# Optimization experiments

Measured on AMD Instinct MI355X. Metric: run time of the kernel, lower is better.

## Reference

```python
import jax, jax.numpy as jnp
import numpy as np

NUM_HEADS = 8
GROUP_SIZE = 4
INF = 1000000.0


def _group(x, mask, g):
    # x: [N, L, D] -> [N, L//g, D] (mean over group); mask: any over group
    N, L, D = x.shape
    xg = x.reshape(N, L // g, g, D).mean(axis=2)
    mg = mask.reshape(N, L // g, g).any(axis=2)
    return xg, mg


def _heads(x, h):
    N, L, D = x.shape
    return x.reshape(N, L, h, D // h)


def _alpha(logits, mask_row, mask_col):
    # logits: [N, L1, L2, H]; masks: [N, L1], [N, L2] (same across heads)
    pair = (mask_row[:, :, None] & mask_col[:, None, :])[..., None]  # [N,L1,L2,1]
    logits = jnp.where(pair, logits, logits - INF)
    alpha = jax.nn.softmax(logits, axis=2)
    return jnp.where(mask_row[:, :, None, None], alpha, jnp.zeros_like(alpha))


def setup_inputs() -> dict:
    key = jax.random.key(0)
    ks = jax.random.split(key, 9)
    N, Lp, Ls, D = 32, 4096, 1024, 256
    protein = jax.random.normal(ks[0], (N, Lp, D), dtype=jnp.float32)
    sm = jax.random.normal(ks[1], (N, Ls, D), dtype=jnp.float32)
    mask_prot = jax.random.randint(ks[2], (N, Lp), 0, 2) > 0
    mask_sm = jax.random.randint(ks[3], (N, Ls), 0, 2) > 0
    scale = 1.0 / np.sqrt(D)
    Wk_p = jax.random.normal(ks[4], (D, D), dtype=jnp.float32) * scale
    Wv_p = jax.random.normal(ks[5], (D, D), dtype=jnp.float32) * scale
    Wq_d = jax.random.normal(ks[6], (D, D), dtype=jnp.float32) * scale
    Wk_d = jax.random.normal(ks[7], (D, D), dtype=jnp.float32) * scale
    Wv_d = jax.random.normal(ks[8], (D, D), dtype=jnp.float32) * scale
    return {"protein": protein, "sm": sm, "mask_prot": mask_prot,
            "mask_sm": mask_sm, "Wk_p": Wk_p, "Wv_p": Wv_p,
            "Wq_d": Wq_d, "Wk_d": Wk_d, "Wv_d": Wv_d}


def reference(protein, sm, mask_prot, mask_sm, Wk_p, Wv_p, Wq_d, Wk_d, Wv_d):
    H = NUM_HEADS
    prot_g, mprot_g = _group(protein, mask_prot, GROUP_SIZE)
    sm_g, msm_g = _group(sm, mask_sm, GROUP_SIZE)

    key_prot = _heads(prot_g @ Wk_p, H)   # [N, Gp, H, d]
    val_prot = _heads(prot_g @ Wv_p, H)
    query_sm = _heads(sm_g @ Wq_d, H)     # [N, Gs, H, d]
    key_sm = _heads(sm_g @ Wk_d, H)
    val_sm = _heads(sm_g @ Wv_d, H)

    logits_dp = jnp.einsum('blhd,bkhd->blkh', query_sm, key_prot)
    logits_dd = jnp.einsum('blhd,bkhd->blkh', query_sm, key_sm)

    alpha_dp = _alpha(logits_dp, msm_g, mprot_g)
    alpha_dd = _alpha(logits_dd, msm_g, msm_g)

    out_dp = jnp.einsum('blkh,bkhd->blhd', alpha_dp, val_prot)
    out_dd = jnp.einsum('blkh,bkhd->blhd', alpha_dd, val_sm)
    N, Gs = out_dp.shape[0], out_dp.shape[1]
    return (out_dp.reshape(N, Gs, -1) + out_dd.reshape(N, Gs, -1)) * 0.5
```

## Files before the change

### kernel.cpp

```cpp
#include <hip/hip_runtime.h>
#include <cstdint>
#include <cstddef>

#define N_B 32
#define D_MODEL 256
#define H_N 8
#define HD 32
#define GP 1024
#define GS 256
#define LOG2E 1.4426950408889634f

typedef __attribute__((ext_vector_type(8))) _Float16 half8;
typedef __attribute__((ext_vector_type(4))) float floatx4;

#if __has_builtin(__builtin_amdgcn_exp2f)
#define EXP2(x) __builtin_amdgcn_exp2f(x)
#else
#define EXP2(x) exp2f(x)
#endif

__device__ __forceinline__ unsigned short f2h(float f) {
    _Float16 h = (_Float16)f;
    return __builtin_bit_cast(unsigned short, h);
}

__device__ __forceinline__ unsigned pack_h_rne(float a, float b) {
    return (unsigned)f2h(a) | ((unsigned)f2h(b) << 16);
}

#define PRO_A (N_B * GP * 64)
#define PRO_B (N_B * GS * 64)
#define PRO_C (N_B * GP)
#define PRO_D (N_B * GS)
#define PRO_BLOCKS ((PRO_A + PRO_B + PRO_C + PRO_D) / 256)
#define WT_BLOCKS 80
__global__ __launch_bounds__(256) void prologue_w(
        const float4* __restrict__ prot, const float4* __restrict__ smx,
        const int* __restrict__ mp, const int* __restrict__ ms,
        ushort4* __restrict__ prot_g, ushort4* __restrict__ sm_g,
        float* __restrict__ bias_p, float* __restrict__ bias_s,
        const float* __restrict__ Wk_p, const float* __restrict__ Wv_p,
        const float* __restrict__ Wq_d, const float* __restrict__ Wk_d,
        const float* __restrict__ Wv_d,
        unsigned short* __restrict__ WTbig, unsigned short* __restrict__ WTsml) {
    __shared__ unsigned short sT[64 * 65];
    int blk = blockIdx.x;
    int t = threadIdx.x;
    if (blk >= WT_BLOCKS) {
        int gid = (blk - WT_BLOCKS) * 256 + t;
        if (gid < PRO_A + PRO_B) {
            const float4* x; ushort4* xg; int g2;
            if (gid < PRO_A) { x = prot; xg = prot_g; g2 = gid; }
            else { x = smx; xg = sm_g; g2 = gid - PRO_A; }
            int row = g2 >> 6, c = g2 & 63;
            const float4* p = x + (size_t)row * 256 + c;
            float4 a = p[0], b = p[64], cc = p[128], d = p[192];
            ushort4 r;
            r.x = f2h(0.25f * (a.x + b.x + cc.x + d.x));
            r.y = f2h(0.25f * (a.y + b.y + cc.y + d.y));
            r.z = f2h(0.25f * (a.z + b.z + cc.z + d.z));
            r.w = f2h(0.25f * (a.w + b.w + cc.w + d.w));
            xg[g2] = r;
        } else {
            int g2 = gid - (PRO_A + PRO_B);
            const int* m; float* bias;
            if (g2 < PRO_C) { m = mp; bias = bias_p; }
            else { m = ms; bias = bias_s; g2 -= PRO_C; }
            const int* p = m + (size_t)g2 * 4;
            bias[g2] = (p[0] | p[1] | p[2] | p[3]) ? 0.0f : -1442695.0f;
        }
    } else {
        int wb = blk;
        int y = wb >> 4, bx = wb & 15;
        const float* W; unsigned short* WT; int pidx;
        if (y < 2) { W = (y == 0) ? Wk_p : Wv_p; WT = WTbig; pidx = y; }
        else {
            int q = y - 2;
            W = (q == 0) ? Wq_d : (q == 1 ? Wk_d : Wv_d);
            WT = WTsml; pidx = q;
        }
        int kt = bx >> 2, ct = bx & 3;
        int k0 = kt * 64, c0 = ct * 64;
#pragma unroll
        for (int j = 0; j < 4; j++) {
            int idx = j * 256 + t;
            int kr = idx >> 4, cf = idx & 15;
            float4 v = *(const float4*)&W[(size_t)(k0 + kr) * 256 + c0 + cf * 4];
            sT[(cf * 4 + 0) * 65 + kr] = f2h(v.x);
            sT[(cf * 4 + 1) * 65 + kr] = f2h(v.y);
            sT[(cf * 4 + 2) * 65 + kr] = f2h(v.z);
            sT[(cf * 4 + 3) * 65 + kr] = f2h(v.w);
        }
        __syncthreads();
#pragma unroll
        for (int j = 0; j < 8; j++) {
            int idx = j * 256 + t;
            int cw = idx >> 5, kq = idx & 31;
            unsigned lo = sT[cw * 65 + kq * 2];
            unsigned hi = sT[cw * 65 + kq * 2 + 1];
            ((unsigned*)WT)[((size_t)pidx * 256 + c0 + cw) * 128 + (k0 >> 1) + kq] =
                lo | (hi << 16);
        }
    }
}

__global__ __launch_bounds__(256) void gemm_f16(
        const unsigned short* __restrict__ Abig,
        const unsigned short* __restrict__ WTbig,
        const unsigned short* __restrict__ Asml,
        const unsigned short* __restrict__ WTsml,
        unsigned short* __restrict__ Kp, unsigned short* __restrict__ Vpt,
        unsigned short* __restrict__ Qd, unsigned short* __restrict__ Ksd,
        unsigned short* __restrict__ Vsdt) {
    __shared__ alignas(16) unsigned short lds[128 * 128];
    unsigned short* As = lds;
    unsigned short* Bs = lds + 8192;

    int bid = blockIdx.x;
    int id = (bid & 7) * 176 + (bid >> 3);

    const unsigned short *A, *WT;
    unsigned short *oK0, *oK1, *oV;
    int Gg, lgG, row0, col0;
    float scale0;
    bool isV;
    if (id < 1024) {
        A = Abig; WT = WTbig; oK0 = Kp; oK1 = Kp; oV = Vpt;
        Gg = GP; lgG = 10; scale0 = 1.0f;
        col0 = (id & 3) << 7; row0 = (id >> 2) << 7;
        isV = (col0 >= 256);
    } else {
        int tq = id - 1024;
        A = Asml; WT = WTsml; oK0 = Qd; oK1 = Ksd; oV = Vsdt;
        Gg = GS; lgG = 8; scale0 = LOG2E;
        col0 = (tq % 6) << 7; row0 = (tq / 6) << 7;
        isV = (col0 >= 512);
    }
    const int tid = threadIdx.x;
    const int ln = tid & 63, wave = tid >> 6;
    const int m16 = ln & 15, quad = ln >> 4;
    const int wm = (wave & 1) * 64, wn = (wave >> 1) * 64;

    const uint4* gA[4];
    const uint4* gB[4];
    unsigned ldsoff[4];
#pragma unroll
    for (int j = 0; j < 4; j++) {
        int u = (j * 4 + wave) * 64 + ln;
        int r = u >> 3, s = u & 7;
        int sg = (s - r) & 7;
        gA[j] = (const uint4*)A + (size_t)(row0 + r) * 32 + sg;
        gB[j] = (const uint4*)WT + (size_t)(col0 + r) * 32 + sg;
        ldsoff[j] = (unsigned)((j * 4 + wave) * 512);
    }
    int aaddr[4], baddr[4];
#pragma unroll
    for (int i = 0; i < 4; i++) {
        int rA = wm + i * 16 + m16;
        aaddr[i] = rA * 128 + ((quad + rA) & 7) * 16;
        int rB = wn + i * 16 + m16;
        baddr[i] = rB * 128 + ((quad + rB) & 7) * 16;
    }

    floatx4 acc[4][4] = {};
    for (int ko = 0; ko < 32; ko += 8) {
        __syncthreads();
#pragma unroll
        for (int j = 0; j < 4; j++) {
            __builtin_amdgcn_global_load_lds(
                (const __attribute__((address_space(1))) void*)(gA[j] + ko),
                (__attribute__((address_space(3))) void*)&As[ldsoff[j]], 16, 0, 0);
            __builtin_amdgcn_global_load_lds(
                (const __attribute__((address_space(1))) void*)(gB[j] + ko),
                (__attribute__((address_space(3))) void*)&Bs[ldsoff[j]], 16, 0, 0);
        }
        __syncthreads();
#pragma unroll
        for (int kh = 0; kh < 2; kh++) {
            half8 af[4], bfr[4];
#pragma unroll
            for (int i = 0; i < 4; i++) {
                af[i]  = *(const half8*)((const char*)As + (aaddr[i] ^ (kh << 6)));
                bfr[i] = *(const half8*)((const char*)Bs + (baddr[i] ^ (kh << 6)));
            }
#pragma unroll
            for (int im = 0; im < 4; im++)
#pragma unroll
                for (int in = 0; in < 4; in++)
                    acc[im][in] = __builtin_amdgcn_mfma_f32_16x16x32_f16(
                        af[im], bfr[in], acc[im][in], 0, 0, 0);
        }
    }

    if (!isV) {
#pragma unroll
        for (int im = 0; im < 4; im++) {
#pragma unroll
            for (int in = 0; in < 4; in++) {
                int colg = col0 + wn + in * 16 + m16;
                int p = colg >> 8, h = (colg >> 5) & 7, d = colg & 31;
                unsigned short* ob = (p == 0) ? oK0 : oK1;
                float sc = (p == 0) ? scale0 : 1.0f;
#pragma unroll
                for (int r = 0; r < 4; r++) {
                    int Mrow = row0 + wm + im * 16 + quad * 4 + r;
                    int nb = Mrow >> lgG, g = Mrow & (Gg - 1);
                    ob[(((size_t)nb * 8 + h) * Gg + g) * 32 + d] =
                        f2h(acc[im][in][r] * sc);
                }
            }
        }
    } else {
        __syncthreads();
#pragma unroll
        for (int in = 0; in < 4; in++) {
            int col = wn + in * 16 + m16;
            unsigned cb = (unsigned)col * 128;
            unsigned swz = (unsigned)((col & 15) << 3);
#pragma unroll
            for (int imp = 0; imp < 2; imp++) {
#pragma unroll
                for (int r = 0; r < 4; r++) {
                    unsigned pos = (unsigned)(wm + imp * 32 + 8 * quad + 2 * r);
                    *(unsigned*)&lds[cb + (pos ^ swz)] =
                        pack_h_rne(acc[2 * imp][in][r], acc[2 * imp + 1][in][r]);
                }
            }
        }
        __syncthreads();
        int nb = row0 >> lgG;
        int kbase = row0 & (Gg - 1);
        const int tcol = tid >> 4, p8 = tid & 15;
#pragma unroll
        for (int j = 0; j < 8; j++) {
            int col = j * 16 + tcol;
            int colg = col0 + col;
            int h = (colg >> 5) & 7, d = colg & 31;
            uint4 v = *(const uint4*)&lds[col * 128 + ((p8 * 8) ^ ((col & 15) << 3))];
            *(uint4*)(oV + (((size_t)nb * 8 + h) * 32 + d) * Gg + kbase + p8 * 8) = v;
        }
    }
}

struct KVFrag { uint4 k0, k1, v0, v1; float b0, b1; };

__device__ __forceinline__ KVFrag load_frag(
        const uint4* K4, const uint4* V4, const float* bias,
        int c, int Gk8, int m16, int quad) {
    KVFrag f;
    f.k0 = K4[(c * 32 + m16) * 4 + quad];
    f.k1 = K4[(c * 32 + 16 + m16) * 4 + quad];
    f.v0 = V4[(size_t)m16 * Gk8 + c * 4 + quad];
    f.v1 = V4[(size_t)(16 + m16) * Gk8 + c * 4 + quad];
    f.b0 = bias[c * 32 + m16];
    f.b1 = bias[c * 32 + 16 + m16];
    return f;
}

__device__ __forceinline__ void attn_stream(
        const unsigned short* __restrict__ Kb,
        const unsigned short* __restrict__ Vtb,
        const float* __restrict__ bias, int Lk,
        half8 qfA, half8 qfB, unsigned* sPw,
        int m16, int quad, float* lA, float* lB,
        floatx4& oA0, floatx4& oA1, floatx4& oB0, floatx4& oB1) {
    const uint4* K4 = (const uint4*)Kb;
    const uint4* V4 = (const uint4*)Vtb;
    const int Gk8 = Lk >> 3;
    const int nchunks = Lk >> 5;
    KVFrag cur = load_frag(K4, V4, bias, 0, Gk8, m16, quad);
    for (int c = 0; c < nchunks; c++) {
        int cn = (c + 1 < nchunks) ? c + 1 : c;
        KVFrag nxt = load_frag(K4, V4, bias, cn, Gk8, m16, quad);
        union { uint4 u; half8 v; } t0, t1, pA, pB;
        t0.u = cur.k0; t1.u = cur.k1;
        floatx4 z = {0.f, 0.f, 0.f, 0.f};
        __builtin_amdgcn_s_setprio(1);
        floatx4 sA0 = __builtin_amdgcn_mfma_f32_16x16x32_f16(qfA, t0.v, z, 0, 0, 0);
        floatx4 sA1 = __builtin_amdgcn_mfma_f32_16x16x32_f16(qfA, t1.v, z, 0, 0, 0);
        floatx4 sB0 = __builtin_amdgcn_mfma_f32_16x16x32_f16(qfB, t0.v, z, 0, 0, 0);
        floatx4 sB1 = __builtin_amdgcn_mfma_f32_16x16x32_f16(qfB, t1.v, z, 0, 0, 0);
        __builtin_amdgcn_s_setprio(0);
#pragma unroll
        for (int r = 0; r < 4; r++) {
            _Float16 hA0 = (_Float16)EXP2(sA0[r] + cur.b0);
            _Float16 hA1 = (_Float16)EXP2(sA1[r] + cur.b1);
            _Float16 hB0 = (_Float16)EXP2(sB0[r] + cur.b0);
            _Float16 hB1 = (_Float16)EXP2(sB1[r] + cur.b1);
            lA[r] += (float)hA0 + (float)hA1;
            lB[r] += (float)hB0 + (float)hB1;
            unsigned uA = (unsigned)__builtin_bit_cast(unsigned short, hA0) |
                          ((unsigned)__builtin_bit_cast(unsigned short, hA1) << 16);
            unsigned uB = (unsigned)__builtin_bit_cast(unsigned short, hB0) |
                          ((unsigned)__builtin_bit_cast(unsigned short, hB1) << 16);
            sPw[(quad * 4 + r) * 20 + m16] = uA;
            sPw[320 + (quad * 4 + r) * 20 + m16] = uB;
        }
        pA.u = *(const uint4*)&sPw[m16 * 20 + quad * 4];
        pB.u = *(const uint4*)&sPw[320 + m16 * 20 + quad * 4];
        t0.u = cur.v0; t1.u = cur.v1;
        __builtin_amdgcn_s_setprio(1);
        oA0 = __builtin_amdgcn_mfma_f32_16x16x32_f16(pA.v, t0.v, oA0, 0, 0, 0);
        oA1 = __builtin_amdgcn_mfma_f32_16x16x32_f16(pA.v, t1.v, oA1, 0, 0, 0);
        oB0 = __builtin_amdgcn_mfma_f32_16x16x32_f16(pB.v, t0.v, oB0, 0, 0, 0);
        oB1 = __builtin_amdgcn_mfma_f32_16x16x32_f16(pB.v, t1.v, oB1, 0, 0, 0);
        __builtin_amdgcn_s_setprio(0);
        cur = nxt;
    }
}

__global__ __launch_bounds__(512) void attn_mfma(
        const unsigned short* __restrict__ Qd, const unsigned short* __restrict__ Kp,
        const unsigned short* __restrict__ Vpt, const unsigned short* __restrict__ Ksd,
        const unsigned short* __restrict__ Vsdt, const float* __restrict__ bias_p,
        const float* __restrict__ bias_s, float* __restrict__ out) {
    __shared__ alignas(16) unsigned sP[8][640];
    const int b = blockIdx.x;
    const int n = b >> 3, h = b & 7;
    const int tid = threadIdx.x, wave = tid >> 6, ln = tid & 63;
    const int m16 = ln & 15, quad = ln >> 4;
    const int q0 = wave * 32;
    unsigned* sPw = sP[wave];

    union { uint4 u; half8 v; } qfA, qfB;
    qfA.u = ((const uint4*)Qd)[(((size_t)n * 8 + h) * GS + q0 + m16) * 4 + quad];
    qfB.u = ((const uint4*)Qd)[(((size_t)n * 8 + h) * GS + q0 + 16 + m16) * 4 + quad];

    float lAdp[4] = {0, 0, 0, 0}, lBdp[4] = {0, 0, 0, 0};
    float lAdd[4] = {0, 0, 0, 0}, lBdd[4] = {0, 0, 0, 0};
    floatx4 oAdp0 = {}, oAdp1 = {}, oBdp0 = {}, oBdp1 = {};
    floatx4 oAdd0 = {}, oAdd1 = {}, oBdd0 = {}, oBdd1 = {};

    attn_stream(Kp + ((size_t)n * 8 + h) * GP * 32,
                Vpt + ((size_t)n * 8 + h) * GP * 32,
                bias_p + (size_t)n * GP, GP, qfA.v, qfB.v, sPw, m16, quad,
                lAdp, lBdp, oAdp0, oAdp1, oBdp0, oBdp1);
    attn_stream(Ksd + ((size_t)n * 8 + h) * GS * 32,
                Vsdt + ((size_t)n * 8 + h) * GS * 32,
                bias_s + (size_t)n * GS, GS, qfA.v, qfB.v, sPw, m16, quad,
                lAdd, lBdd, oAdd0, oAdd1, oBdd0, oBdd1);

#pragma unroll
    for (int r = 0; r < 4; r++) {
#pragma unroll
        for (int off = 1; off < 16; off <<= 1) {
            lAdp[r] += __shfl_xor(lAdp[r], off, 64);
            lBdp[r] += __shfl_xor(lBdp[r], off, 64);
            lAdd[r] += __shfl_xor(lAdd[r], off, 64);
            lBdd[r] += __shfl_xor(lBdd[r], off, 64);
        }
    }
#pragma unroll
    for (int r = 0; r < 4; r++) {
        int qrowA = q0 + quad * 4 + r;
        bool rmA = (bias_s[(size_t)n * GS + qrowA] == 0.0f);
        float idpA = 1.f / lAdp[r], iddA = 1.f / lAdd[r];
        float* obA = out + ((size_t)n * GS + qrowA) * 256 + h * 32;
        obA[m16]      = rmA ? 0.5f * (oAdp0[r] * idpA + oAdd0[r] * iddA) : 0.f;
        obA[16 + m16] = rmA ? 0.5f * (oAdp1[r] * idpA + oAdd1[r] * iddA) : 0.f;
        int qrowB = q0 + 16 + quad * 4 + r;
        bool rmB = (bias_s[(size_t)n * GS + qrowB] == 0.0f);
        float idpB = 1.f / lBdp[r], iddB = 1.f / lBdd[r];
        float* obB = out + ((size_t)n * GS + qrowB) * 256 + h * 32;
        obB[m16]      = rmB ? 0.5f * (oBdp0[r] * idpB + oBdd0[r] * iddB) : 0.f;
        obB[16 + m16] = rmB ? 0.5f * (oBdp1[r] * idpB + oBdd1[r] * iddB) : 0.f;
    }
}

extern "C" void kernel_launch(void* const* d_in, const int* in_sizes, int n_in,
                              void* d_out, int out_size, void* d_ws,
                              size_t ws_size, hipStream_t stream) {
    const float* protein   = (const float*)d_in[0];
    const float* smx       = (const float*)d_in[1];
    const int*   mask_prot = (const int*)d_in[2];
    const int*   mask_sm   = (const int*)d_in[3];
    const float* Wk_p = (const float*)d_in[4];
    const float* Wv_p = (const float*)d_in[5];
    const float* Wq_d = (const float*)d_in[6];
    const float* Wk_d = (const float*)d_in[7];
    const float* Wv_d = (const float*)d_in[8];
    float* out = (float*)d_out;

    char* ws = (char*)d_ws;
    unsigned short* prot_g = (unsigned short*)ws; ws += (size_t)N_B * GP * 256 * 2;
    unsigned short* sm_g   = (unsigned short*)ws; ws += (size_t)N_B * GS * 256 * 2;
    unsigned short* WTbig  = (unsigned short*)ws; ws += (size_t)512 * 256 * 2;
    unsigned short* WTsml  = (unsigned short*)ws; ws += (size_t)768 * 256 * 2;
    unsigned short* Kp     = (unsigned short*)ws; ws += (size_t)N_B * H_N * GP * 32 * 2;
    unsigned short* Vpt    = (unsigned short*)ws; ws += (size_t)N_B * H_N * GP * 32 * 2;
    unsigned short* Qd     = (unsigned short*)ws; ws += (size_t)N_B * H_N * GS * 32 * 2;
    unsigned short* Ksd    = (unsigned short*)ws; ws += (size_t)N_B * H_N * GS * 32 * 2;
    unsigned short* Vsdt   = (unsigned short*)ws; ws += (size_t)N_B * H_N * GS * 32 * 2;
    float* bias_p = (float*)ws; ws += (size_t)N_B * GP * 4;
    float* bias_s = (float*)ws; ws += (size_t)N_B * GS * 4;

    prologue_w<<<PRO_BLOCKS + WT_BLOCKS, 256, 0, stream>>>(
        (const float4*)protein, (const float4*)smx, mask_prot, mask_sm,
        (ushort4*)prot_g, (ushort4*)sm_g, bias_p, bias_s,
        Wk_p, Wv_p, Wq_d, Wk_d, Wv_d, WTbig, WTsml);

    gemm_f16<<<1024 + 384, 256, 0, stream>>>(
        prot_g, WTbig, sm_g, WTsml, Kp, Vpt, Qd, Ksd, Vsdt);

    attn_mfma<<<N_B * H_N, 512, 0, stream>>>(Qd, Kp, Vpt, Ksd, Vsdt,
                                             bias_p, bias_s, out);
}
```

Baseline: 278.8 us.

## Fuse group-mean and fp16 conversion into GEMM A-tile loading

```diff
diff --git a/kernel.cpp b/kernel.cpp
--- a/kernel.cpp
+++ b/kernel.cpp
@@ -28,16 +28,12 @@
     return (unsigned)f2h(a) | ((unsigned)f2h(b) << 16);
 }
 
-#define PRO_A (N_B * GP * 64)
-#define PRO_B (N_B * GS * 64)
 #define PRO_C (N_B * GP)
 #define PRO_D (N_B * GS)
-#define PRO_BLOCKS ((PRO_A + PRO_B + PRO_C + PRO_D) / 256)
+#define MASK_BLOCKS ((PRO_C + PRO_D) / 256)
 #define WT_BLOCKS 80
 __global__ __launch_bounds__(256) void prologue_w(
-        const float4* __restrict__ prot, const float4* __restrict__ smx,
         const int* __restrict__ mp, const int* __restrict__ ms,
-        ushort4* __restrict__ prot_g, ushort4* __restrict__ sm_g,
         float* __restrict__ bias_p, float* __restrict__ bias_s,
         const float* __restrict__ Wk_p, const float* __restrict__ Wv_p,
         const float* __restrict__ Wq_d, const float* __restrict__ Wk_d,
@@ -47,28 +43,12 @@
     int blk = blockIdx.x;
     int t = threadIdx.x;
     if (blk >= WT_BLOCKS) {
-        int gid = (blk - WT_BLOCKS) * 256 + t;
-        if (gid < PRO_A + PRO_B) {
-            const float4* x; ushort4* xg; int g2;
-            if (gid < PRO_A) { x = prot; xg = prot_g; g2 = gid; }
-            else { x = smx; xg = sm_g; g2 = gid - PRO_A; }
-            int row = g2 >> 6, c = g2 & 63;
-            const float4* p = x + (size_t)row * 256 + c;
-            float4 a = p[0], b = p[64], cc = p[128], d = p[192];
-            ushort4 r;
-            r.x = f2h(0.25f * (a.x + b.x + cc.x + d.x));
-            r.y = f2h(0.25f * (a.y + b.y + cc.y + d.y));
-            r.z = f2h(0.25f * (a.z + b.z + cc.z + d.z));
-            r.w = f2h(0.25f * (a.w + b.w + cc.w + d.w));
-            xg[g2] = r;
-        } else {
-            int g2 = gid - (PRO_A + PRO_B);
-            const int* m; float* bias;
-            if (g2 < PRO_C) { m = mp; bias = bias_p; }
-            else { m = ms; bias = bias_s; g2 -= PRO_C; }
-            const int* p = m + (size_t)g2 * 4;
-            bias[g2] = (p[0] | p[1] | p[2] | p[3]) ? 0.0f : -1442695.0f;
-        }
+        int g2 = (blk - WT_BLOCKS) * 256 + t;
+        const int* m; float* bias;
+        if (g2 < PRO_C) { m = mp; bias = bias_p; }
+        else { m = ms; bias = bias_s; g2 -= PRO_C; }
+        const int* p = m + (size_t)g2 * 4;
+        bias[g2] = (p[0] | p[1] | p[2] | p[3]) ? 0.0f : -1442695.0f;
     } else {
         int wb = blk;
         int y = wb >> 4, bx = wb & 15;
@@ -105,9 +85,9 @@
 }
 
 __global__ __launch_bounds__(256) void gemm_f16(
-        const unsigned short* __restrict__ Abig,
+        const float* __restrict__ Abig,
         const unsigned short* __restrict__ WTbig,
-        const unsigned short* __restrict__ Asml,
+        const float* __restrict__ Asml,
         const unsigned short* __restrict__ WTsml,
         unsigned short* __restrict__ Kp, unsigned short* __restrict__ Vpt,
         unsigned short* __restrict__ Qd, unsigned short* __restrict__ Ksd,
@@ -119,7 +99,8 @@
     int bid = blockIdx.x;
     int id = (bid & 7) * 176 + (bid >> 3);
 
-    const unsigned short *A, *WT;
+    const float* A;
+    const unsigned short* WT;
     unsigned short *oK0, *oK1, *oV;
     int Gg, lgG, row0, col0;
     float scale0;
@@ -141,7 +122,7 @@
     const int m16 = ln & 15, quad = ln >> 4;
     const int wm = (wave & 1) * 64, wn = (wave >> 1) * 64;
 
-    const uint4* gA[4];
+    const float4* gA[4];
     const uint4* gB[4];
     unsigned ldsoff[4];
 #pragma unroll
@@ -149,7 +130,7 @@
         int u = (j * 4 + wave) * 64 + ln;
         int r = u >> 3, s = u & 7;
         int sg = (s - r) & 7;
-        gA[j] = (const uint4*)A + (size_t)(row0 + r) * 32 + sg;
+        gA[j] = (const float4*)A + (size_t)(row0 + r) * 256 + 2 * sg;
         gB[j] = (const uint4*)WT + (size_t)(col0 + r) * 32 + sg;
         ldsoff[j] = (unsigned)((j * 4 + wave) * 512);
     }
@@ -168,11 +149,23 @@
 #pragma unroll
         for (int j = 0; j < 4; j++) {
             __builtin_amdgcn_global_load_lds(
-                (const __attribute__((address_space(1))) void*)(gA[j] + ko),
-                (__attribute__((address_space(3))) void*)&As[ldsoff[j]], 16, 0, 0);
-            __builtin_amdgcn_global_load_lds(
                 (const __attribute__((address_space(1))) void*)(gB[j] + ko),
                 (__attribute__((address_space(3))) void*)&Bs[ldsoff[j]], 16, 0, 0);
+            const float4* g = gA[j] + 2 * ko;
+            float4 a0 = g[0],   a1 = g[1];
+            float4 b0 = g[64],  b1 = g[65];
+            float4 c0 = g[128], c1 = g[129];
+            float4 d0 = g[192], d1 = g[193];
+            uint4 w;
+            w.x = pack_h_rne(0.25f * (a0.x + b0.x + c0.x + d0.x),
+                             0.25f * (a0.y + b0.y + c0.y + d0.y));
+            w.y = pack_h_rne(0.25f * (a0.z + b0.z + c0.z + d0.z),
+                             0.25f * (a0.w + b0.w + c0.w + d0.w));
+            w.z = pack_h_rne(0.25f * (a1.x + b1.x + c1.x + d1.x),
+                             0.25f * (a1.y + b1.y + c1.y + d1.y));
+            w.w = pack_h_rne(0.25f * (a1.z + b1.z + c1.z + d1.z),
+                             0.25f * (a1.w + b1.w + c1.w + d1.w));
+            *(uint4*)&As[ldsoff[j] + (unsigned)ln * 8] = w;
         }
         __syncthreads();
 #pragma unroll
@@ -382,8 +375,6 @@
     float* out = (float*)d_out;
 
     char* ws = (char*)d_ws;
-    unsigned short* prot_g = (unsigned short*)ws; ws += (size_t)N_B * GP * 256 * 2;
-    unsigned short* sm_g   = (unsigned short*)ws; ws += (size_t)N_B * GS * 256 * 2;
     unsigned short* WTbig  = (unsigned short*)ws; ws += (size_t)512 * 256 * 2;
     unsigned short* WTsml  = (unsigned short*)ws; ws += (size_t)768 * 256 * 2;
     unsigned short* Kp     = (unsigned short*)ws; ws += (size_t)N_B * H_N * GP * 32 * 2;
@@ -394,13 +385,12 @@
     float* bias_p = (float*)ws; ws += (size_t)N_B * GP * 4;
     float* bias_s = (float*)ws; ws += (size_t)N_B * GS * 4;
 
-    prologue_w<<<PRO_BLOCKS + WT_BLOCKS, 256, 0, stream>>>(
-        (const float4*)protein, (const float4*)smx, mask_prot, mask_sm,
-        (ushort4*)prot_g, (ushort4*)sm_g, bias_p, bias_s,
+    prologue_w<<<WT_BLOCKS + MASK_BLOCKS, 256, 0, stream>>>(
+        mask_prot, mask_sm, bias_p, bias_s,
         Wk_p, Wv_p, Wq_d, Wk_d, Wv_d, WTbig, WTsml);
 
     gemm_f16<<<1024 + 384, 256, 0, stream>>>(
-        prot_g, WTbig, sm_g, WTsml, Kp, Vpt, Qd, Ksd, Vsdt);
+        protein, WTbig, smx, WTsml, Kp, Vpt, Qd, Ksd, Vsdt);
 
     attn_mfma<<<N_B * H_N, 512, 0, stream>>>(Qd, Kp, Vpt, Ksd, Vsdt,
                                              bias_p, bias_s, out);
```

Result: slower. 299.2 us (+7.3%).
